# Kernel tuning notes

Hardware: AMD Instinct MI355X
Metric: run time of the kernel (lower is better)

## Reference

```python
import jax, jax.numpy as jnp
import numpy as np

B, L, S, H, E = 2, 2048, 2048, 8, 64
MASK_SCALE = 10000.0
TAU_MIN, TAU_MAX = 0.1, 5.0
THR_MIN, THR_MAX = 0.01, 0.99


def setup_inputs() -> dict:
    key = jax.random.key(0)
    ks = jax.random.split(key, 7)
    query = jax.random.normal(ks[0], (B, L, H, E), jnp.float32)
    k_ = jax.random.normal(ks[1], (B, S, H, E), jnp.float32)
    value = jax.random.normal(ks[2], (B, S, H, E), jnp.float32)
    mask_miss_k = jnp.zeros((B, S), jnp.float32)  # unused in forward
    mask_miss_q = jnp.zeros((B, L), jnp.float32)  # unused in forward
    pos = jnp.arange(B * L, dtype=jnp.int32).reshape(B, L, 1)  # monotone positions per batch
    hard_mask = jax.random.randint(ks[3], (L, S), 0, 2, dtype=jnp.int32)
    hard_mask = hard_mask.at[jnp.arange(L), jnp.arange(S)].set(1)  # keep diagonal open
    # learned parameters / stochastic state
    phi = jax.random.normal(ks[4], (H, L, S), jnp.float32)  # DAG edge logits (per head)
    log_tau_gs = jnp.asarray(np.log(2.0), jnp.float32)
    threshold = jnp.asarray(0.5, jnp.float32)
    u = jax.random.uniform(ks[5], (H, L, S), jnp.float32, 1e-6, 1.0 - 1e-6)  # Gumbel base noise
    return {"query": query, "key": k_, "value": value, "mask_miss_k": mask_miss_k,
            "mask_miss_q": mask_miss_q, "pos": pos, "causal_mask": 1,
            "hard_mask": hard_mask, "phi": phi, "log_tau_gs": log_tau_gs,
            "threshold": threshold, "u": u}


def reference(query, key, value, mask_miss_k, mask_miss_q, pos, causal_mask,
              hard_mask, phi, log_tau_gs, threshold, u):
    e = query.shape[-1]
    scale = 1.0 / np.sqrt(e)
    # scores: (B, H, L, S)
    scores = jnp.einsum('blhe,bshe->bhls', query, key)
    if causal_mask:
        p = pos[..., 0]  # (B, L)
        causal = jnp.where(p[:, None, :] > p[:, :, None], -jnp.inf, 0.0).astype(scores.dtype)
        scores = scores + causal[:, None, :, :]
    # Gumbel-sigmoid relaxed DAG mask
    tau = jnp.clip(jnp.exp(log_tau_gs), TAU_MIN, TAU_MAX)
    gumbel = jnp.log(u + 1e-8) - jnp.log(1.0 - u + 1e-8)
    m_relaxed = jax.nn.sigmoid((gumbel + phi) / tau)  # (H, L, S)
    thr = jnp.clip(threshold, THR_MIN, THR_MAX)
    dag_add = MASK_SCALE * jnp.minimum(m_relaxed - thr, 0.0)  # <=0 additive penalty
    scores = scores + dag_add[None, :, :, :]
    # hard mask applied pre-softmax as -inf
    scores = jnp.where(hard_mask[None, None, :, :] == 0, -jnp.inf, scores)
    att = jax.nn.softmax(scale * scores, axis=-1)  # dropout p=0 (eval)
    out = jnp.einsum('bhls,bshe->blhe', att, value)  # (B, L, H, E)
    return out
```

## Files before the change

kernel.cpp:

```cpp
#include <hip/hip_runtime.h>
#include <hip/hip_fp16.h>


#define Bz 2
#define Lz 2048
#define Sz 2048
#define Hz 8
#define Ez 64
#define NSEG 4
#define NEG_BIG (-1e30f)

typedef __attribute__((ext_vector_type(8))) short short8;
typedef __attribute__((ext_vector_type(4))) short short4v;
typedef __attribute__((ext_vector_type(4))) float f32x4;

__device__ __forceinline__ float fast_rcp(float x) { return __builtin_amdgcn_rcpf(x); }

__device__ __forceinline__ short f2bf(float x) {
    unsigned bits = __builtin_bit_cast(unsigned, x);
    bits += 0x7FFFu + ((bits >> 16) & 1u);
    return (short)(bits >> 16);
}

__device__ __forceinline__ int tri_prefix(int lt) {
    const int m = lt >> 2;
    return lt + 2*m*(m-1) + (lt & 3)*m;
}

__global__ void pack_qk(const float* __restrict__ q, const float* __restrict__ k,
                        short* __restrict__ qp, short* __restrict__ kp,
                        const int* __restrict__ hm, const int* __restrict__ caus_p,
                        unsigned long long* __restrict__ dmask)
{
    const int t = blockIdx.x * 256 + threadIdx.x;
    const float4 qv = ((const float4*)q)[t];
    const float4 kv = ((const float4*)k)[t];
    const int e4   = t & 15;
    const int rest = t >> 4;
    const int h    = rest & 7;
    const int bl   = rest >> 3;
    const int b    = bl >> 11;
    const int l    = bl & 2047;
    const int o    = ((b*Hz + h)*Lz + l)*Ez + e4*4;
    short4v qo, ko;
    qo[0] = f2bf(qv.x*0.125f); qo[1] = f2bf(qv.y*0.125f);
    qo[2] = f2bf(qv.z*0.125f); qo[3] = f2bf(qv.w*0.125f);
    ko[0] = f2bf(kv.x); ko[1] = f2bf(kv.y); ko[2] = f2bf(kv.z); ko[3] = f2bf(kv.w);
    *(short4v*)&qp[o] = qo;
    *(short4v*)&kp[o] = ko;

    {
        const int lane = threadIdx.x & 63;
        const int lrow = blockIdx.x;
        const int w0   = (threadIdx.x >> 6) * 8;
        const int causal = *caus_p;
#pragma unroll
        for (int i = 0; i < 8; ++i) {
            const int tt = w0 + i;
            int dead;
            if (causal && (tt*64 > lrow)) {
                dead = 1;
            } else {
                const int s = tt*64 + lane;
                dead = (hm[lrow*Sz + s] == 0) || (causal && (s > lrow));
            }
            const unsigned long long m = __ballot(dead);
            if (lane == 0) dmask[lrow*32 + tt] = m;
        }
    }
}

__global__ void pack_vt(const float* __restrict__ v, short* __restrict__ vt)
{
    const int blk = blockIdx.x;
    const int st  = blk & 63;
    const int h   = (blk >> 6) & 7;
    const int b   = blk >> 9;
    const int s0  = st * 32;
    const int e   = threadIdx.x & 63;
    const int sc  = threadIdx.x >> 6;
    short8 ov;
#pragma unroll
    for (int j = 0; j < 8; ++j) {
        const int s = s0 + sc*8 + j;
        ov[j] = f2bf(v[((b*Sz + s)*Hz + h)*Ez + e]);
    }
    *(short8*)&vt[((b*Hz + h)*Ez + e)*Sz + s0 + sc*8] = ov;
}

__global__ __launch_bounds__(256) void dg_gen(
    const float* __restrict__ phi, const float* __restrict__ u,
    const unsigned long long* __restrict__ dmask, const int* __restrict__ caus_p,
    const float* __restrict__ log_tau_p, const float* __restrict__ thr_p,
    unsigned short* __restrict__ dgp)
{
    const int lane  = threadIdx.x & 63;
    const int wslot = threadIdx.x >> 6;
    const int h     = blockIdx.x & 7;
    const int lt    = 127 - (blockIdx.x >> 3);
    const int quad  = lane >> 4;
    const int ln    = lane & 15;

    const int causal = *caus_p;
    float tau = __expf(*log_tau_p);
    tau = fminf(fmaxf(tau, 0.1f), 5.0f);
    const float inv_tau = 1.0f / tau;
    const float thr = fminf(fmaxf(*thr_p, 0.01f), 0.99f);

    const int C  = lt >> 2;
    const int Tg = causal ? (C + 1) : (Sz >> 6);
    const int tb = causal ? (h*2112 + tri_prefix(lt)) : (h*128 + lt)*32;

    __shared__ float myd_all[4][16*68];
    float* myd = myd_all[wslot];

    for (int t = wslot; t < Tg; t += 4) {
        unsigned long long dmc[4];
        f32x4 pv[4], uv[4];
#pragma unroll
        for (int i = 0; i < 4; ++i) {
            const int l = lt*16 + quad*4 + i;
            const size_t off = ((size_t)(h*Lz + l))*Sz + (size_t)(t*64 + ln*4);
            pv[i]  = *(const f32x4*)&phi[off];
            uv[i]  = *(const f32x4*)&u[off];
            dmc[i] = dmask[l*32 + t];
        }
#pragma unroll
        for (int i = 0; i < 4; ++i) {
            f32x4 dv;
#pragma unroll
            for (int cc = 0; cc < 4; ++cc) {
                const float uvv = uv[i][cc];
                const float g   = __logf((uvv + 1e-8f) * fast_rcp(1.0f - uvv + 1e-8f));
                const float z   = (g + pv[i][cc]) * inv_tau;
                const float sg  = fast_rcp(1.0f + __expf(-z));
                const float d   = 1250.0f * fminf(sg - thr, 0.0f);
                const bool dead = (dmc[i] >> (ln*4 + cc)) & 1ull;
                dv[cc] = dead ? -INFINITY : d;
            }
            *(f32x4*)&myd[(quad*4 + i)*68 + ln*4] = dv;
        }
        asm volatile("s_waitcnt lgkmcnt(0)" ::: "memory");
        __builtin_amdgcn_sched_barrier(0);

        unsigned out[8];
#pragma unroll
        for (int r = 0; r < 4; ++r) {
            const float v0 = myd[(quad*4 + r)*68 +  0 + ln];
            const float v1 = myd[(quad*4 + r)*68 + 16 + ln];
            const float v2 = myd[(quad*4 + r)*68 + 32 + ln];
            const float v3 = myd[(quad*4 + r)*68 + 48 + ln];
            out[r*2]   = (unsigned)__half_as_ushort(__float2half(v0))
                       | ((unsigned)__half_as_ushort(__float2half(v1)) << 16);
            out[r*2+1] = (unsigned)__half_as_ushort(__float2half(v2))
                       | ((unsigned)__half_as_ushort(__float2half(v3)) << 16);
        }
        const size_t o16 = ((size_t)(tb + t) << 10) + (size_t)lane*16;
        uint4 w0, w1;
        w0.x = out[0]; w0.y = out[1]; w0.z = out[2]; w0.w = out[3];
        w1.x = out[4]; w1.y = out[5]; w1.z = out[6]; w1.w = out[7];
        *(uint4*)&dgp[o16]     = w0;
        *(uint4*)&dgp[o16 + 8] = w1;
    }
}

__global__ __launch_bounds__(256, 3) void attn_main(
    const unsigned short* __restrict__ dgp, const int* __restrict__ causal_p,
    const short* __restrict__ qp, const short* __restrict__ kp,
    const short* __restrict__ vt,
    float* __restrict__ Op, float* __restrict__ Mp, float* __restrict__ Lp)
{
    const int lane  = threadIdx.x & 63;
    const int wslot = threadIdx.x >> 6;
    const int qq    = blockIdx.x;
    const int seg   = qq & 3;
    const int cc    = qq >> 2;
    const int h     = cc & 7;
    const int C     = 31 - (cc >> 3);
    const int l_base = C*64 + wslot*16;
    const int ln    = lane & 15;
    const int quad  = lane >> 4;

    const int causal = *causal_p;
    const int lt = C*4 + wslot;
    const int tb = causal ? (h*2112 + tri_prefix(lt)) : (h*128 + lt)*32;
    const int T  = causal ? (C + 1) : (Sz >> 6);

    f32x4 O[2][4];
    float m_r[2][4], l_r[2][4];
#pragma unroll
    for (int b = 0; b < 2; ++b) {
#pragma unroll
        for (int ne = 0; ne < 4; ++ne) { f32x4 z = {0.f,0.f,0.f,0.f}; O[b][ne] = z; }
#pragma unroll
        for (int r = 0; r < 4; ++r) { m_r[b][r] = -INFINITY; l_r[b][r] = 0.f; }
    }

    __shared__ __align__(16) short plds[4][16*72];
    short* myp = &plds[wslot][0];

    for (int t = seg; t < T; t += NSEG) {
        const int s0 = t << 6;

        const size_t doff = ((size_t)(tb + t) << 10) + (size_t)lane*16;
        const uint4 dA = *(const uint4*)&dgp[doff];
        const uint4 dB = *(const uint4*)&dgp[doff + 8];

        float dgf[4][4];

#pragma unroll
        for (int b = 0; b < 2; ++b) {
            short8 qfb[2];
#pragma unroll
            for (int k = 0; k < 2; ++k)
                qfb[k] = *(const short8*)&qp[((b*Hz + h)*Lz + l_base + ln)*Ez + k*32 + quad*8];
            short8 kf[4][2];
#pragma unroll
            for (int nt = 0; nt < 4; ++nt)
#pragma unroll
                for (int k = 0; k < 2; ++k)
                    kf[nt][k] = *(const short8*)&kp[((b*Hz + h)*Sz + s0 + nt*16 + ln)*Ez + k*32 + quad*8];
            short8 vv[4][2];
#pragma unroll
            for (int ne = 0; ne < 4; ++ne) {
                vv[ne][0] = *(const short8*)&vt[((b*Hz + h)*Ez + ne*16 + ln)*Sz + s0 + quad*8];
                vv[ne][1] = *(const short8*)&vt[((b*Hz + h)*Ez + ne*16 + ln)*Sz + s0 + 32 + quad*8];
            }

            if (b == 0) {
#pragma unroll
                for (int r = 0; r < 4; ++r) {
                    const unsigned dw0 = (r < 2) ? (&dA.x)[r*2]     : (&dB.x)[(r-2)*2];
                    const unsigned dw1 = (r < 2) ? (&dA.x)[r*2 + 1] : (&dB.x)[(r-2)*2 + 1];
                    dgf[0][r] = __half2float(__ushort_as_half((unsigned short)(dw0 & 0xffffu)));
                    dgf[1][r] = __half2float(__ushort_as_half((unsigned short)(dw0 >> 16)));
                    dgf[2][r] = __half2float(__ushort_as_half((unsigned short)(dw1 & 0xffffu)));
                    dgf[3][r] = __half2float(__ushort_as_half((unsigned short)(dw1 >> 16)));
                }
            }

            f32x4 Sc[4];
#pragma unroll
            for (int nt = 0; nt < 4; ++nt) {
                f32x4 z4 = {0.f,0.f,0.f,0.f};
                z4 = __builtin_amdgcn_mfma_f32_16x16x32_bf16(qfb[0], kf[nt][0], z4, 0, 0, 0);
                Sc[nt] = __builtin_amdgcn_mfma_f32_16x16x32_bf16(qfb[1], kf[nt][1], z4, 0, 0, 0);
            }

            float mx[4];
#pragma unroll
            for (int r = 0; r < 4; ++r) mx[r] = -INFINITY;
#pragma unroll
            for (int nt = 0; nt < 4; ++nt)
#pragma unroll
                for (int r = 0; r < 4; ++r) {
                    Sc[nt][r] += dgf[nt][r];
                    mx[r] = fmaxf(mx[r], Sc[nt][r]);
                }
#pragma unroll
            for (int r = 0; r < 4; ++r)
#pragma unroll
                for (int o = 1; o < 16; o <<= 1)
                    mx[r] = fmaxf(mx[r], __shfl_xor(mx[r], o, 16));

            float al[4], mn[4];
#pragma unroll
            for (int r = 0; r < 4; ++r) {
                mn[r] = fmaxf(m_r[b][r], mx[r]);
                al[r] = __expf(fmaxf(m_r[b][r], NEG_BIG) - fmaxf(mn[r], NEG_BIG));
                m_r[b][r] = mn[r];
            }

            float ps[4] = {0.f, 0.f, 0.f, 0.f};
#pragma unroll
            for (int nt = 0; nt < 4; ++nt)
#pragma unroll
                for (int r = 0; r < 4; ++r) {
                    const float p = __expf(Sc[nt][r] - fmaxf(mn[r], NEG_BIG));
                    ps[r] += p;
                    myp[(quad*4 + r)*72 + nt*16 + ln] = f2bf(p);
                }
#pragma unroll
            for (int r = 0; r < 4; ++r) {
#pragma unroll
                for (int o = 1; o < 16; o <<= 1)
                    ps[r] += __shfl_xor(ps[r], o, 16);
                l_r[b][r] = l_r[b][r] * al[r] + ps[r];
            }
#pragma unroll
            for (int ne = 0; ne < 4; ++ne)
#pragma unroll
                for (int r = 0; r < 4; ++r)
                    O[b][ne][r] *= al[r];

            short8 pa[2];
#pragma unroll
            for (int k = 0; k < 2; ++k)
                pa[k] = *(const short8*)&myp[ln*72 + k*32 + quad*8];

#pragma unroll
            for (int ne = 0; ne < 4; ++ne) {
                O[b][ne] = __builtin_amdgcn_mfma_f32_16x16x32_bf16(pa[0], vv[ne][0], O[b][ne], 0, 0, 0);
                O[b][ne] = __builtin_amdgcn_mfma_f32_16x16x32_bf16(pa[1], vv[ne][1], O[b][ne], 0, 0, 0);
            }
        }
    }

#pragma unroll
    for (int b = 0; b < 2; ++b) {
#pragma unroll
        for (int ne = 0; ne < 4; ++ne)
#pragma unroll
            for (int r = 0; r < 4; ++r) {
                const int l = l_base + quad*4 + r;
                Op[(((seg*2 + b)*Hz + h)*Lz + l)*Ez + ne*16 + ln] = O[b][ne][r];
            }
        if (ln == 0) {
#pragma unroll
            for (int r = 0; r < 4; ++r) {
                const int l = l_base + quad*4 + r;
                Mp[((seg*2 + b)*Hz + h)*Lz + l] = m_r[b][r];
                Lp[((seg*2 + b)*Hz + h)*Lz + l] = l_r[b][r];
            }
        }
    }
}

__global__ void merge_k(const float* __restrict__ Op, const float* __restrict__ Mp,
                        const float* __restrict__ Lp, float* __restrict__ out)
{
    const int t = blockIdx.x * 256 + threadIdx.x;
    const int e4   = (t & 15) * 4;
    const int rest = t >> 4;
    const int h    = rest & 7;
    const int bl   = rest >> 3;
    const int b    = bl >> 11;
    const int l    = bl & 2047;

    float ms[NSEG], ls[NSEG], m = -INFINITY;
#pragma unroll
    for (int s = 0; s < NSEG; ++s) {
        const int idx = ((s*2 + b)*Hz + h)*Lz + l;
        ms[s] = Mp[idx];
        ls[s] = Lp[idx];
        m = fmaxf(m, ms[s]);
    }
    const float mg = fmaxf(m, NEG_BIG);
    float den = 0.f, a0 = 0.f, a1 = 0.f, a2 = 0.f, a3 = 0.f;
#pragma unroll
    for (int s = 0; s < NSEG; ++s) {
        const float w = __expf(fmaxf(ms[s], NEG_BIG) - mg);
        den += w * ls[s];
        const float4 ov = *(const float4*)&Op[(((s*2 + b)*Hz + h)*Lz + l)*Ez + e4];
        a0 += w * ov.x; a1 += w * ov.y; a2 += w * ov.z; a3 += w * ov.w;
    }
    const float rd = 1.0f / den;
    float4 res;
    res.x = a0 * rd; res.y = a1 * rd; res.z = a2 * rd; res.w = a3 * rd;
    *(float4*)&out[((b*Lz + l)*Hz + h)*Ez + e4] = res;
}

extern "C" void kernel_launch(void* const* d_in, const int* in_sizes, int n_in,
                              void* d_out, int out_size, void* d_ws, size_t ws_size,
                              hipStream_t stream)
{
    const float* q     = (const float*)d_in[0];
    const float* k     = (const float*)d_in[1];
    const float* v     = (const float*)d_in[2];
    const int*   caus  = (const int*)d_in[6];
    const int*   hm    = (const int*)d_in[7];
    const float* phi   = (const float*)d_in[8];
    const float* ltau  = (const float*)d_in[9];
    const float* thr   = (const float*)d_in[10];
    const float* u     = (const float*)d_in[11];

    char* ws = (char*)d_ws;
    short* qp = (short*)(ws);
    short* kp = (short*)(ws + (size_t)( 4u << 20));
    short* vt = (short*)(ws + (size_t)( 8u << 20));
    float* Op = (float*)(ws + (size_t)(12u << 20));
    float* Mp = (float*)(ws + (size_t)(44u << 20));
    float* Lp = (float*)(ws + (size_t)(44u << 20) + (512u << 10));
    unsigned long long* dmask = (unsigned long long*)(ws + (size_t)(45u << 20));
    unsigned short* dgp = (unsigned short*)(ws + (size_t)(46u << 20));

    pack_qk <<<2048, 256, 0, stream>>>(q, k, qp, kp, hm, caus, dmask);
    pack_vt <<<1024, 256, 0, stream>>>(v, vt);
    dg_gen  <<<1024, 256, 0, stream>>>(phi, u, dmask, caus, ltau, thr, dgp);
    attn_main<<<1024, 256, 0, stream>>>(dgp, caus, qp, kp, vt, Op, Mp, Lp);
    merge_k <<<2048, 256, 0, stream>>>(Op, Mp, Lp, (float*)d_out);
}
```

Measured before the change: 396.8 us.

## Fuse pack and DAG-mask generation into one prep kernel, drop dmask bitmask

Merges the three preprocessing kernels (Q/K pack, V transpose, DAG penalty generation) into a single launch that dispatches on block index. The dead-mask bitmask pass is removed: the DAG generator now reads hard_mask directly as int4 vectors and computes causality inline. This removes two launches and the dmask write/read round trip, but it makes the DAG blocks read full hard_mask rows per head (8x redundant across heads) and mixes heterogeneous blocks in one grid.

```diff
diff --git a/kernel.cpp b/kernel.cpp
--- a/kernel.cpp
+++ b/kernel.cpp
@@ -27,140 +27,128 @@
     return lt + 2*m*(m-1) + (lt & 3)*m;
 }
 
-__global__ void pack_qk(const float* __restrict__ q, const float* __restrict__ k,
-                        short* __restrict__ qp, short* __restrict__ kp,
-                        const int* __restrict__ hm, const int* __restrict__ caus_p,
-                        unsigned long long* __restrict__ dmask)
-{
-    const int t = blockIdx.x * 256 + threadIdx.x;
-    const float4 qv = ((const float4*)q)[t];
-    const float4 kv = ((const float4*)k)[t];
-    const int e4   = t & 15;
-    const int rest = t >> 4;
-    const int h    = rest & 7;
-    const int bl   = rest >> 3;
-    const int b    = bl >> 11;
-    const int l    = bl & 2047;
-    const int o    = ((b*Hz + h)*Lz + l)*Ez + e4*4;
-    short4v qo, ko;
-    qo[0] = f2bf(qv.x*0.125f); qo[1] = f2bf(qv.y*0.125f);
-    qo[2] = f2bf(qv.z*0.125f); qo[3] = f2bf(qv.w*0.125f);
-    ko[0] = f2bf(kv.x); ko[1] = f2bf(kv.y); ko[2] = f2bf(kv.z); ko[3] = f2bf(kv.w);
-    *(short4v*)&qp[o] = qo;
-    *(short4v*)&kp[o] = ko;
-
-    {
-        const int lane = threadIdx.x & 63;
-        const int lrow = blockIdx.x;
-        const int w0   = (threadIdx.x >> 6) * 8;
-        const int causal = *caus_p;
-#pragma unroll
-        for (int i = 0; i < 8; ++i) {
-            const int tt = w0 + i;
-            int dead;
-            if (causal && (tt*64 > lrow)) {
-                dead = 1;
-            } else {
-                const int s = tt*64 + lane;
-                dead = (hm[lrow*Sz + s] == 0) || (causal && (s > lrow));
-            }
-            const unsigned long long m = __ballot(dead);
-            if (lane == 0) dmask[lrow*32 + tt] = m;
-        }
-    }
-}
-
-__global__ void pack_vt(const float* __restrict__ v, short* __restrict__ vt)
+__global__ __launch_bounds__(256) void prep(
+    const float* __restrict__ q, const float* __restrict__ k,
+    const float* __restrict__ v,
+    const float* __restrict__ phi, const float* __restrict__ u,
+    const int* __restrict__ hm, const int* __restrict__ caus_p,
+    const float* __restrict__ log_tau_p, const float* __restrict__ thr_p,
+    short* __restrict__ qp, short* __restrict__ kp, short* __restrict__ vt,
+    unsigned short* __restrict__ dgp)
 {
     const int blk = blockIdx.x;
-    const int st  = blk & 63;
-    const int h   = (blk >> 6) & 7;
-    const int b   = blk >> 9;
-    const int s0  = st * 32;
-    const int e   = threadIdx.x & 63;
-    const int sc  = threadIdx.x >> 6;
-    short8 ov;
-#pragma unroll
-    for (int j = 0; j < 8; ++j) {
-        const int s = s0 + sc*8 + j;
-        ov[j] = f2bf(v[((b*Sz + s)*Hz + h)*Ez + e]);
-    }
-    *(short8*)&vt[((b*Hz + h)*Ez + e)*Sz + s0 + sc*8] = ov;
-}
-
-__global__ __launch_bounds__(256) void dg_gen(
-    const float* __restrict__ phi, const float* __restrict__ u,
-    const unsigned long long* __restrict__ dmask, const int* __restrict__ caus_p,
-    const float* __restrict__ log_tau_p, const float* __restrict__ thr_p,
-    unsigned short* __restrict__ dgp)
-{
-    const int lane  = threadIdx.x & 63;
-    const int wslot = threadIdx.x >> 6;
-    const int h     = blockIdx.x & 7;
-    const int lt    = 127 - (blockIdx.x >> 3);
-    const int quad  = lane >> 4;
-    const int ln    = lane & 15;
-
-    const int causal = *caus_p;
-    float tau = __expf(*log_tau_p);
-    tau = fminf(fmaxf(tau, 0.1f), 5.0f);
-    const float inv_tau = 1.0f / tau;
-    const float thr = fminf(fmaxf(*thr_p, 0.01f), 0.99f);
-
-    const int C  = lt >> 2;
-    const int Tg = causal ? (C + 1) : (Sz >> 6);
-    const int tb = causal ? (h*2112 + tri_prefix(lt)) : (h*128 + lt)*32;
-
-    __shared__ float myd_all[4][16*68];
-    float* myd = myd_all[wslot];
-
-    for (int t = wslot; t < Tg; t += 4) {
-        unsigned long long dmc[4];
-        f32x4 pv[4], uv[4];
-#pragma unroll
-        for (int i = 0; i < 4; ++i) {
-            const int l = lt*16 + quad*4 + i;
-            const size_t off = ((size_t)(h*Lz + l))*Sz + (size_t)(t*64 + ln*4);
-            pv[i]  = *(const f32x4*)&phi[off];
-            uv[i]  = *(const f32x4*)&u[off];
-            dmc[i] = dmask[l*32 + t];
+
+    if (blk < 2048) {
+        const int t = blk * 256 + threadIdx.x;
+        const float4 qv = ((const float4*)q)[t];
+        const float4 kv = ((const float4*)k)[t];
+        const int e4   = t & 15;
+        const int rest = t >> 4;
+        const int h    = rest & 7;
+        const int bl   = rest >> 3;
+        const int b    = bl >> 11;
+        const int l    = bl & 2047;
+        const int o    = ((b*Hz + h)*Lz + l)*Ez + e4*4;
+        short4v qo, ko;
+        qo[0] = f2bf(qv.x*0.125f); qo[1] = f2bf(qv.y*0.125f);
+        qo[2] = f2bf(qv.z*0.125f); qo[3] = f2bf(qv.w*0.125f);
+        ko[0] = f2bf(kv.x); ko[1] = f2bf(kv.y); ko[2] = f2bf(kv.z); ko[3] = f2bf(kv.w);
+        *(short4v*)&qp[o] = qo;
+        *(short4v*)&kp[o] = ko;
+        return;
+    }
+
+    if (blk < 3072) {
+        const int bk  = blk - 2048;
+        const int st  = bk & 63;
+        const int h   = (bk >> 6) & 7;
+        const int b   = bk >> 9;
+        const int s0  = st * 32;
+        const int e   = threadIdx.x & 63;
+        const int sc  = threadIdx.x >> 6;
+        short8 ov;
+#pragma unroll
+        for (int j = 0; j < 8; ++j) {
+            const int s = s0 + sc*8 + j;
+            ov[j] = f2bf(v[((b*Sz + s)*Hz + h)*Ez + e]);
         }
-#pragma unroll
-        for (int i = 0; i < 4; ++i) {
-            f32x4 dv;
-#pragma unroll
-            for (int cc = 0; cc < 4; ++cc) {
-                const float uvv = uv[i][cc];
-                const float g   = __logf((uvv + 1e-8f) * fast_rcp(1.0f - uvv + 1e-8f));
-                const float z   = (g + pv[i][cc]) * inv_tau;
-                const float sg  = fast_rcp(1.0f + __expf(-z));
-                const float d   = 1250.0f * fminf(sg - thr, 0.0f);
-                const bool dead = (dmc[i] >> (ln*4 + cc)) & 1ull;
-                dv[cc] = dead ? -INFINITY : d;
-            }
-            *(f32x4*)&myd[(quad*4 + i)*68 + ln*4] = dv;
+        *(short8*)&vt[((b*Hz + h)*Ez + e)*Sz + s0 + sc*8] = ov;
+        return;
+    }
+
+    {
+        const int bk    = blk - 3072;
+        const int lane  = threadIdx.x & 63;
+        const int wslot = threadIdx.x >> 6;
+        const int h     = bk & 7;
+        const int lt    = 127 - (bk >> 3);
+        const int quad  = lane >> 4;
+        const int ln    = lane & 15;
+
+        const int causal = *caus_p;
+        float tau = __expf(*log_tau_p);
+        tau = fminf(fmaxf(tau, 0.1f), 5.0f);
+        const float inv_tau = 1.0f / tau;
+        const float thr = fminf(fmaxf(*thr_p, 0.01f), 0.99f);
+
+        const int C  = lt >> 2;
+        const int Tg = causal ? (C + 1) : (Sz >> 6);
+        const int tb = causal ? (h*2112 + tri_prefix(lt)) : (h*128 + lt)*32;
+
+        __shared__ float myd_all[4][16*68];
+        float* myd = myd_all[wslot];
+
+        for (int t = wslot; t < Tg; t += 4) {
+            f32x4 pv[4], uv[4];
+            int4  hm4[4];
+#pragma unroll
+            for (int i = 0; i < 4; ++i) {
+                const int l = lt*16 + quad*4 + i;
+                const size_t off = ((size_t)(h*Lz + l))*Sz + (size_t)(t*64 + ln*4);
+                pv[i]  = *(const f32x4*)&phi[off];
+                uv[i]  = *(const f32x4*)&u[off];
+                hm4[i] = *(const int4*)&hm[l*Sz + t*64 + ln*4];
+            }
+#pragma unroll
+            for (int i = 0; i < 4; ++i) {
+                const int l = lt*16 + quad*4 + i;
+                f32x4 dv;
+#pragma unroll
+                for (int cc = 0; cc < 4; ++cc) {
+                    const float uvv = uv[i][cc];
+                    const float g   = __logf((uvv + 1e-8f) * fast_rcp(1.0f - uvv + 1e-8f));
+                    const float z   = (g + pv[i][cc]) * inv_tau;
+                    const float sg  = fast_rcp(1.0f + __expf(-z));
+                    const float d   = 1250.0f * fminf(sg - thr, 0.0f);
+                    const int s     = t*64 + ln*4 + cc;
+                    const int hmv   = (&hm4[i].x)[cc];
+                    const bool dead = (hmv == 0) || (causal && (s > l));
+                    dv[cc] = dead ? -INFINITY : d;
+                }
+                *(f32x4*)&myd[(quad*4 + i)*68 + ln*4] = dv;
+            }
+            asm volatile("s_waitcnt lgkmcnt(0)" ::: "memory");
+            __builtin_amdgcn_sched_barrier(0);
+
+            unsigned out[8];
+#pragma unroll
+            for (int r = 0; r < 4; ++r) {
+                const float v0 = myd[(quad*4 + r)*68 +  0 + ln];
+                const float v1 = myd[(quad*4 + r)*68 + 16 + ln];
+                const float v2 = myd[(quad*4 + r)*68 + 32 + ln];
+                const float v3 = myd[(quad*4 + r)*68 + 48 + ln];
+                out[r*2]   = (unsigned)__half_as_ushort(__float2half(v0))
+                           | ((unsigned)__half_as_ushort(__float2half(v1)) << 16);
+                out[r*2+1] = (unsigned)__half_as_ushort(__float2half(v2))
+                           | ((unsigned)__half_as_ushort(__float2half(v3)) << 16);
+            }
+            const size_t o16 = ((size_t)(tb + t) << 10) + (size_t)lane*16;
+            uint4 w0, w1;
+            w0.x = out[0]; w0.y = out[1]; w0.z = out[2]; w0.w = out[3];
+            w1.x = out[4]; w1.y = out[5]; w1.z = out[6]; w1.w = out[7];
+            *(uint4*)&dgp[o16]     = w0;
+            *(uint4*)&dgp[o16 + 8] = w1;
         }
-        asm volatile("s_waitcnt lgkmcnt(0)" ::: "memory");
-        __builtin_amdgcn_sched_barrier(0);
-
-        unsigned out[8];
-#pragma unroll
-        for (int r = 0; r < 4; ++r) {
-            const float v0 = myd[(quad*4 + r)*68 +  0 + ln];
-            const float v1 = myd[(quad*4 + r)*68 + 16 + ln];
-            const float v2 = myd[(quad*4 + r)*68 + 32 + ln];
-            const float v3 = myd[(quad*4 + r)*68 + 48 + ln];
-            out[r*2]   = (unsigned)__half_as_ushort(__float2half(v0))
-                       | ((unsigned)__half_as_ushort(__float2half(v1)) << 16);
-            out[r*2+1] = (unsigned)__half_as_ushort(__float2half(v2))
-                       | ((unsigned)__half_as_ushort(__float2half(v3)) << 16);
-        }
-        const size_t o16 = ((size_t)(tb + t) << 10) + (size_t)lane*16;
-        uint4 w0, w1;
-        w0.x = out[0]; w0.y = out[1]; w0.z = out[2]; w0.w = out[3];
-        w1.x = out[4]; w1.y = out[5]; w1.z = out[6]; w1.w = out[7];
-        *(uint4*)&dgp[o16]     = w0;
-        *(uint4*)&dgp[o16 + 8] = w1;
     }
 }
 
@@ -381,12 +369,10 @@
     float* Op = (float*)(ws + (size_t)(12u << 20));
     float* Mp = (float*)(ws + (size_t)(44u << 20));
     float* Lp = (float*)(ws + (size_t)(44u << 20) + (512u << 10));
-    unsigned long long* dmask = (unsigned long long*)(ws + (size_t)(45u << 20));
     unsigned short* dgp = (unsigned short*)(ws + (size_t)(46u << 20));
 
-    pack_qk <<<2048, 256, 0, stream>>>(q, k, qp, kp, hm, caus, dmask);
-    pack_vt <<<1024, 256, 0, stream>>>(v, vt);
-    dg_gen  <<<1024, 256, 0, stream>>>(phi, u, dmask, caus, ltau, thr, dgp);
+    prep     <<<4096, 256, 0, stream>>>(q, k, v, phi, u, hm, caus, ltau, thr,
+                                        qp, kp, vt, dgp);
     attn_main<<<1024, 256, 0, stream>>>(dgp, caus, qp, kp, vt, Op, Mp, Lp);
-    merge_k <<<2048, 256, 0, stream>>>(Op, Mp, Lp, (float*)d_out);
-}
+    merge_k  <<<2048, 256, 0, stream>>>(Op, Mp, Lp, (float*)d_out);
+}
```

Result: no change. 394.8 us (-0.5%).
